# Optimization experiments

Hardware: AMD Instinct MI355X
Metric: run time of the kernel (lower is better)

Reference implementation:

```python
import jax, jax.numpy as jnp
import numpy as np

N_NODES = 100000
N_EDGES = 1600000
HIDDEN = 256
CONV_OUT = 128
OUT = 2


def setup_inputs() -> dict:
    key = jax.random.key(0)
    k1, k2, k3, k4, k5, k6, k7 = jax.random.split(key, 7)
    x = jax.random.normal(k1, (N_NODES, HIDDEN), dtype=jnp.float32)
    edge_index = jax.random.randint(k2, (2, N_EDGES), 0, N_NODES, dtype=jnp.int64)
    edge_weight = jax.random.uniform(k3, (N_EDGES,), dtype=jnp.float32)
    # GCNConv parameters (lin: hidden->128, bias added after aggregation)
    W1 = jax.random.normal(k4, (HIDDEN, CONV_OUT), dtype=jnp.float32) / np.sqrt(HIDDEN)
    b1 = jnp.zeros((CONV_OUT,), dtype=jnp.float32)
    # head Linear(128, out_channels)
    W2 = jax.random.normal(k5, (CONV_OUT, OUT), dtype=jnp.float32) / np.sqrt(CONV_OUT)
    b2 = jax.random.normal(k6, (OUT,), dtype=jnp.float32) * 0.01
    return {"x": x, "edge_index": edge_index, "edge_weight": edge_weight,
            "W1": W1, "b1": b1, "W2": W2, "b2": b2}


def reference(x, edge_index, edge_weight, W1, b1, W2, b2):
    # GCNConv (use_weights=True branch, no relu), dropout in eval mode (identity), then Linear.
    N = x.shape[0]
    src, dst = edge_index[0], edge_index[1]
    # add self-loops with weight 1 (PyG default fill_value=1.0)
    loop = jnp.arange(N, dtype=src.dtype)
    src = jnp.concatenate([src, loop])
    dst = jnp.concatenate([dst, loop])
    w = jnp.concatenate([edge_weight, jnp.ones((N,), dtype=edge_weight.dtype)])
    # symmetric normalization: norm = d^{-1/2}[src] * w * d^{-1/2}[dst]
    deg = jax.ops.segment_sum(w, dst, num_segments=N)
    dinv = jnp.where(deg > 0, jax.lax.rsqrt(deg), 0.0)
    norm = dinv[src] * w * dinv[dst]
    # transform then gather-scatter aggregate
    h = x @ W1                                   # [N, 128]
    msgs = norm[:, None] * h[src]                # [E+N, 128]
    agg = jax.ops.segment_sum(msgs, dst, num_segments=N) + b1  # [N, 128]
    return agg @ W2 + b2                         # [N, out_channels]
```

## Files before the change

kernel.cpp:

```cpp
#include <hip/hip_runtime.h>

#define N_NODES 100000
#define N_EDGES 1600000
#define HIDDEN 256

#define BSH 7
#define BNODES 128
#define NB 782
#define NPB 256
#define EPB 6250
#define SLOTS 32
#define NZB 12500


__global__ __launch_bounds__(1024) void k_place(
        const int* __restrict__ ei, const float* __restrict__ ew,
        const float* __restrict__ W1, const float* __restrict__ b1,
        const float* __restrict__ W2, const float* __restrict__ b2,
        int* __restrict__ cnt, uint2* __restrict__ rec,
        float* __restrict__ W12, float* __restrict__ cvec) {
    const int tid = threadIdx.x, bid = blockIdx.x;
    if (bid == NPB) {
        if (tid < HIDDEN) {
            const float4* w1r = (const float4*)(W1 + (size_t)tid * 128);
            float a0 = 0.f, a1 = 0.f;
#pragma unroll 8
            for (int k4 = 0; k4 < 32; ++k4) {
                float4 v = w1r[k4];
                a0 += v.x * W2[8 * k4 + 0]; a1 += v.x * W2[8 * k4 + 1];
                a0 += v.y * W2[8 * k4 + 2]; a1 += v.y * W2[8 * k4 + 3];
                a0 += v.z * W2[8 * k4 + 4]; a1 += v.z * W2[8 * k4 + 5];
                a0 += v.w * W2[8 * k4 + 6]; a1 += v.w * W2[8 * k4 + 7];
            }
            W12[2 * tid] = a0; W12[2 * tid + 1] = a1;
            if (tid < 2) {
                float acc = b2[tid];
                for (int k = 0; k < 128; ++k) acc += b1[k] * W2[2 * k + tid];
                cvec[tid] = acc;
            }
        }
        return;
    }
    __shared__ int cursor[NB];
    for (int i = tid; i < NB; i += 1024) cursor[i] = 0;
    __syncthreads();
    const int e0 = bid * EPB, e1 = e0 + EPB;
    for (int e = e0 + tid; e < e1; e += 1024) {
        int d = ei[N_EDGES + e];
        int s = ei[e];
        float wv = ew[e];
        int bk = ((unsigned)d) >> BSH;
        int pos = atomicAdd(&cursor[bk], 1);
        if (pos < SLOTS)
            rec[((size_t)bk * NPB + bid) * SLOTS + pos] =
                make_uint2((unsigned)s | ((unsigned)(d & (BNODES - 1)) << 17),
                           __float_as_uint(wv));
    }
    __syncthreads();
    for (int i = tid; i < NB; i += 1024)
        cnt[(size_t)i * NPB + bid] = min(cursor[i], SLOTS);
}

__global__ __launch_bounds__(256) void k_z(
        const float* __restrict__ x, const float* __restrict__ W12,
        float* __restrict__ z) {
    const int tid = threadIdx.x, lane = tid & 63;
    const float2 w0 = ((const float2*)W12)[lane * 4 + 0];
    const float2 w1 = ((const float2*)W12)[lane * 4 + 1];
    const float2 w2 = ((const float2*)W12)[lane * 4 + 2];
    const float2 w3 = ((const float2*)W12)[lane * 4 + 3];
    const int n0 = (blockIdx.x * 4 + (tid >> 6)) * 2;
    const float4 xa = *(const float4*)(x + (size_t)n0 * HIDDEN + lane * 4);
    const float4 xb = *(const float4*)(x + (size_t)(n0 + 1) * HIDDEN + lane * 4);
    float a0 = xa.x * w0.x + xa.y * w1.x + xa.z * w2.x + xa.w * w3.x;
    float a1 = xa.x * w0.y + xa.y * w1.y + xa.z * w2.y + xa.w * w3.y;
    float c0 = xb.x * w0.x + xb.y * w1.x + xb.z * w2.x + xb.w * w3.x;
    float c1 = xb.x * w0.y + xb.y * w1.y + xb.z * w2.y + xb.w * w3.y;
#pragma unroll
    for (int m = 32; m >= 1; m >>= 1) {
        a0 += __shfl_xor(a0, m, 64);
        a1 += __shfl_xor(a1, m, 64);
        c0 += __shfl_xor(c0, m, 64);
        c1 += __shfl_xor(c1, m, 64);
    }
    if (lane == 0) *(float4*)(z + 2 * n0) = make_float4(a0, a1, c0, c1);
}

__global__ __launch_bounds__(256) void k_deg(
        const uint2* __restrict__ rec, const int* __restrict__ cnt,
        const float* __restrict__ z, float* __restrict__ dinv,
        float2* __restrict__ zn) {
    __shared__ float acc[BNODES];
    const int tid = threadIdx.x, b = blockIdx.x;
    if (tid < BNODES) acc[tid] = 1.0f;
    __syncthreads();
    const int n = cnt[(size_t)b * NPB + tid];
    const uint2* r = rec + ((size_t)b * NPB + tid) * SLOTS;
    for (int i = 0; i < n; ++i) {
        uint2 q = r[i];
        atomicAdd(&acc[q.x >> 17], __uint_as_float(q.y));
    }
    __syncthreads();
    if (tid < BNODES) {
        int node = b * BNODES + tid;
        if (node < N_NODES) {
            float di = rsqrtf(acc[tid]);
            dinv[node] = di;
            float2 zv = ((const float2*)z)[node];
            zn[node] = make_float2(di * zv.x, di * zv.y);
        }
    }
}

__global__ __launch_bounds__(256) void k_gather(
        const uint2* __restrict__ rec, const int* __restrict__ cnt,
        const float* __restrict__ dinv, const float2* __restrict__ zn,
        const float* __restrict__ cvec, float2* __restrict__ out) {
    __shared__ float ax[BNODES], ay[BNODES];
    const int tid = threadIdx.x, b = blockIdx.x;
    if (tid < BNODES) { ax[tid] = 0.f; ay[tid] = 0.f; }
    __syncthreads();
    const int n = cnt[(size_t)b * NPB + tid];
    const uint2* r = rec + ((size_t)b * NPB + tid) * SLOTS;
    for (int i = 0; i < n; ++i) {
        uint2 q = r[i];
        float w = __uint_as_float(q.y);
        float2 s = zn[q.x & 0x1FFFFu];
        int dl = (int)(q.x >> 17);
        atomicAdd(&ax[dl], w * s.x);
        atomicAdd(&ay[dl], w * s.y);
    }
    __syncthreads();
    if (tid < BNODES) {
        int node = b * BNODES + tid;
        if (node < N_NODES) {
            float di = dinv[node];
            float2 s = zn[node];
            out[node] = make_float2(di * ax[tid] + di * s.x + cvec[0],
                                    di * ay[tid] + di * s.y + cvec[1]);
        }
    }
}

extern "C" void kernel_launch(void* const* d_in, const int* in_sizes, int n_in,
                              void* d_out, int out_size, void* d_ws, size_t ws_size,
                              hipStream_t stream) {
    const float* x  = (const float*)d_in[0];
    const int*   ei = (const int*)d_in[1];
    const float* ew = (const float*)d_in[2];
    const float* W1 = (const float*)d_in[3];
    const float* b1 = (const float*)d_in[4];
    const float* W2 = (const float*)d_in[5];
    const float* b2 = (const float*)d_in[6];
    float2* out = (float2*)d_out;

    char* ws = (char*)d_ws;
    uint2*  rec  = (uint2*)ws;           size_t off = (size_t)NB * NPB * SLOTS * 8;
    int*    cnt  = (int*)(ws + off);     off += (size_t)NB * NPB * 4;
    float*  dinv = (float*)(ws + off);   off += (size_t)N_NODES * 4;
    float*  z    = (float*)(ws + off);   off += (size_t)N_NODES * 8;
    float2* zn   = (float2*)(ws + off);  off += (size_t)N_NODES * 8;
    float*  W12  = (float*)(ws + off);   off += HIDDEN * 2 * 4;
    float*  cvec = (float*)(ws + off);   off += 16;

    k_place <<<NPB + 1, 1024, 0, stream>>>(ei, ew, W1, b1, W2, b2, cnt, rec, W12, cvec);
    k_z     <<<NZB, 256, 0, stream>>>(x, W12, z);
    k_deg   <<<NB, 256, 0, stream>>>(rec, cnt, z, dinv, zn);
    k_gather<<<NB, 256, 0, stream>>>(rec, cnt, dinv, zn, cvec, out);
}
```

Measured before the change: 78.65 us.

## Fuse z projection and degree kernels into one launch, apply dinv in gather

Merges the x·W12 projection kernel and the degree-accumulation kernel into a single launch, with the first NB blocks computing degrees and the rest computing z. This removes one kernel launch and the serialization between them. Because dinv is no longer ready when z is written, the pre-scaled zn array is dropped and the gather kernel instead loads dinv[src] per edge and multiplies it in. That adds an extra random 4-byte load per edge in exchange for one fewer launch and no zn pass.

Result: faster. 76.43 us (-2.8%).

```diff
diff --git a/kernel.cpp b/kernel.cpp
--- a/kernel.cpp
+++ b/kernel.cpp
@@ -61,60 +61,53 @@
         cnt[(size_t)i * NPB + bid] = min(cursor[i], SLOTS);
 }
 
-__global__ __launch_bounds__(256) void k_z(
+__global__ __launch_bounds__(256) void k_zdeg(
         const float* __restrict__ x, const float* __restrict__ W12,
-        float* __restrict__ z) {
-    const int tid = threadIdx.x, lane = tid & 63;
-    const float2 w0 = ((const float2*)W12)[lane * 4 + 0];
-    const float2 w1 = ((const float2*)W12)[lane * 4 + 1];
-    const float2 w2 = ((const float2*)W12)[lane * 4 + 2];
-    const float2 w3 = ((const float2*)W12)[lane * 4 + 3];
-    const int n0 = (blockIdx.x * 4 + (tid >> 6)) * 2;
-    const float4 xa = *(const float4*)(x + (size_t)n0 * HIDDEN + lane * 4);
-    const float4 xb = *(const float4*)(x + (size_t)(n0 + 1) * HIDDEN + lane * 4);
-    float a0 = xa.x * w0.x + xa.y * w1.x + xa.z * w2.x + xa.w * w3.x;
-    float a1 = xa.x * w0.y + xa.y * w1.y + xa.z * w2.y + xa.w * w3.y;
-    float c0 = xb.x * w0.x + xb.y * w1.x + xb.z * w2.x + xb.w * w3.x;
-    float c1 = xb.x * w0.y + xb.y * w1.y + xb.z * w2.y + xb.w * w3.y;
+        const uint2* __restrict__ rec, const int* __restrict__ cnt,
+        float* __restrict__ z, float* __restrict__ dinv) {
+    __shared__ float acc[BNODES];
+    const int tid = threadIdx.x, bid = blockIdx.x;
+    if (bid < NB) {
+        if (tid < BNODES) acc[tid] = 1.0f;
+        __syncthreads();
+        const int n = cnt[(size_t)bid * NPB + tid];
+        const uint2* r = rec + ((size_t)bid * NPB + tid) * SLOTS;
+        for (int i = 0; i < n; ++i) {
+            uint2 q = r[i];
+            atomicAdd(&acc[q.x >> 17], __uint_as_float(q.y));
+        }
+        __syncthreads();
+        if (tid < BNODES) {
+            int node = bid * BNODES + tid;
+            if (node < N_NODES) dinv[node] = rsqrtf(acc[tid]);
+        }
+    } else {
+        const int lane = tid & 63;
+        const float2 w0 = ((const float2*)W12)[lane * 4 + 0];
+        const float2 w1 = ((const float2*)W12)[lane * 4 + 1];
+        const float2 w2 = ((const float2*)W12)[lane * 4 + 2];
+        const float2 w3 = ((const float2*)W12)[lane * 4 + 3];
+        const int n0 = (((bid - NB) * 4) + (tid >> 6)) * 2;
+        const float4 xa = *(const float4*)(x + (size_t)n0 * HIDDEN + lane * 4);
+        const float4 xb = *(const float4*)(x + (size_t)(n0 + 1) * HIDDEN + lane * 4);
+        float a0 = xa.x * w0.x + xa.y * w1.x + xa.z * w2.x + xa.w * w3.x;
+        float a1 = xa.x * w0.y + xa.y * w1.y + xa.z * w2.y + xa.w * w3.y;
+        float c0 = xb.x * w0.x + xb.y * w1.x + xb.z * w2.x + xb.w * w3.x;
+        float c1 = xb.x * w0.y + xb.y * w1.y + xb.z * w2.y + xb.w * w3.y;
 #pragma unroll
-    for (int m = 32; m >= 1; m >>= 1) {
-        a0 += __shfl_xor(a0, m, 64);
-        a1 += __shfl_xor(a1, m, 64);
-        c0 += __shfl_xor(c0, m, 64);
-        c1 += __shfl_xor(c1, m, 64);
-    }
-    if (lane == 0) *(float4*)(z + 2 * n0) = make_float4(a0, a1, c0, c1);
-}
-
-__global__ __launch_bounds__(256) void k_deg(
-        const uint2* __restrict__ rec, const int* __restrict__ cnt,
-        const float* __restrict__ z, float* __restrict__ dinv,
-        float2* __restrict__ zn) {
-    __shared__ float acc[BNODES];
-    const int tid = threadIdx.x, b = blockIdx.x;
-    if (tid < BNODES) acc[tid] = 1.0f;
-    __syncthreads();
-    const int n = cnt[(size_t)b * NPB + tid];
-    const uint2* r = rec + ((size_t)b * NPB + tid) * SLOTS;
-    for (int i = 0; i < n; ++i) {
-        uint2 q = r[i];
-        atomicAdd(&acc[q.x >> 17], __uint_as_float(q.y));
-    }
-    __syncthreads();
-    if (tid < BNODES) {
-        int node = b * BNODES + tid;
-        if (node < N_NODES) {
-            float di = rsqrtf(acc[tid]);
-            dinv[node] = di;
-            float2 zv = ((const float2*)z)[node];
-            zn[node] = make_float2(di * zv.x, di * zv.y);
+        for (int m = 32; m >= 1; m >>= 1) {
+            a0 += __shfl_xor(a0, m, 64);
+            a1 += __shfl_xor(a1, m, 64);
+            c0 += __shfl_xor(c0, m, 64);
+            c1 += __shfl_xor(c1, m, 64);
         }
+        if (lane == 0) *(float4*)(z + 2 * n0) = make_float4(a0, a1, c0, c1);
     }
 }
 
 __global__ __launch_bounds__(256) void k_gather(
         const uint2* __restrict__ rec, const int* __restrict__ cnt,
-        const float* __restrict__ dinv, const float2* __restrict__ zn,
+        const float* __restrict__ dinv, const float* __restrict__ z,
         const float* __restrict__ cvec, float2* __restrict__ out) {
     __shared__ float ax[BNODES], ay[BNODES];
     const int tid = threadIdx.x, b = blockIdx.x;
@@ -124,20 +117,21 @@
     const uint2* r = rec + ((size_t)b * NPB + tid) * SLOTS;
     for (int i = 0; i < n; ++i) {
         uint2 q = r[i];
-        float w = __uint_as_float(q.y);
-        float2 s = zn[q.x & 0x1FFFFu];
+        int s = (int)(q.x & 0x1FFFFu);
+        float nw = dinv[s] * __uint_as_float(q.y);
+        float2 zv = ((const float2*)z)[s];
         int dl = (int)(q.x >> 17);
-        atomicAdd(&ax[dl], w * s.x);
-        atomicAdd(&ay[dl], w * s.y);
+        atomicAdd(&ax[dl], nw * zv.x);
+        atomicAdd(&ay[dl], nw * zv.y);
     }
     __syncthreads();
     if (tid < BNODES) {
         int node = b * BNODES + tid;
         if (node < N_NODES) {
             float di = dinv[node];
-            float2 s = zn[node];
-            out[node] = make_float2(di * ax[tid] + di * s.x + cvec[0],
-                                    di * ay[tid] + di * s.y + cvec[1]);
+            float2 zv = ((const float2*)z)[node];
+            out[node] = make_float2(di * ax[tid] + di * di * zv.x + cvec[0],
+                                    di * ay[tid] + di * di * zv.y + cvec[1]);
         }
     }
 }
@@ -159,12 +153,10 @@
     int*    cnt  = (int*)(ws + off);     off += (size_t)NB * NPB * 4;
     float*  dinv = (float*)(ws + off);   off += (size_t)N_NODES * 4;
     float*  z    = (float*)(ws + off);   off += (size_t)N_NODES * 8;
-    float2* zn   = (float2*)(ws + off);  off += (size_t)N_NODES * 8;
     float*  W12  = (float*)(ws + off);   off += HIDDEN * 2 * 4;
     float*  cvec = (float*)(ws + off);   off += 16;
 
     k_place <<<NPB + 1, 1024, 0, stream>>>(ei, ew, W1, b1, W2, b2, cnt, rec, W12, cvec);
-    k_z     <<<NZB, 256, 0, stream>>>(x, W12, z);
-    k_deg   <<<NB, 256, 0, stream>>>(rec, cnt, z, dinv, zn);
-    k_gather<<<NB, 256, 0, stream>>>(rec, cnt, dinv, zn, cvec, out);
+    k_zdeg  <<<NB + NZB, 256, 0, stream>>>(x, W12, rec, cnt, z, dinv);
+    k_gather<<<NB, 256, 0, stream>>>(rec, cnt, dinv, z, cvec, out);
 }
```
